# Kernel optimization log

Hardware: AMD Instinct MI355X
Metric: run time of the kernel (lower is better)

Reference implementation:

```python
import jax, jax.numpy as jnp
import numpy as np

N_AGENTS = 3
OBS_DIM = 30
ACT_DIM = 9
HIDDEN = 128
HEADS = 4
HEAD_DIM = HIDDEN // HEADS
BATCH = 131072
NEG_SLOPE = 0.01
MASK_VAL = -1e10


def _leaky(x):
    return jnp.where(x >= 0, x, NEG_SLOPE * x)


def setup_inputs() -> dict:
    key = jax.random.key(0)
    ks = jax.random.split(key, 20)

    def init(k, shape, fan_in):
        return jax.random.normal(k, shape, dtype=jnp.float32) / np.sqrt(fan_in)

    inp = {
        "observations": jax.random.normal(ks[0], (BATCH, N_AGENTS, OBS_DIM), dtype=jnp.float32),
        "actions": jax.random.uniform(ks[1], (BATCH, N_AGENTS, ACT_DIM), dtype=jnp.float32),
        # per-agent embed weights, stacked over agents: [N, in, out] (already transposed vs torch)
        "W_o": init(ks[2], (N_AGENTS, OBS_DIM, HIDDEN), OBS_DIM),
        "b_o": jnp.zeros((N_AGENTS, HIDDEN), dtype=jnp.float32),
        "W_oa": init(ks[3], (N_AGENTS, OBS_DIM + ACT_DIM, HIDDEN), OBS_DIM + ACT_DIM),
        "b_oa": jnp.zeros((N_AGENTS, HIDDEN), dtype=jnp.float32),
        # shared attention projections: [in, out]
        "Wq": init(ks[4], (HIDDEN, HIDDEN), HIDDEN),
        "bq": jnp.zeros((HIDDEN,), dtype=jnp.float32),
        "Wk": init(ks[5], (HIDDEN, HIDDEN), HIDDEN),
        "bk": jnp.zeros((HIDDEN,), dtype=jnp.float32),
        "Wv": init(ks[6], (HIDDEN, HIDDEN), HIDDEN),
        "bv": jnp.zeros((HIDDEN,), dtype=jnp.float32),
        # per-agent critic MLP: Linear(2H->H) + LeakyReLU + Linear(H->A)
        "Wc1": init(ks[7], (N_AGENTS, 2 * HIDDEN, HIDDEN), 2 * HIDDEN),
        "bc1": jnp.zeros((N_AGENTS, HIDDEN), dtype=jnp.float32),
        "Wc2": init(ks[8], (N_AGENTS, HIDDEN, ACT_DIM), HIDDEN),
        "bc2": jnp.zeros((N_AGENTS, ACT_DIM), dtype=jnp.float32),
    }
    return inp


def reference(observations, actions, W_o, b_o, W_oa, b_oa, Wq, bq, Wk, bk, Wv, bv, Wc1, bc1, Wc2, bc2):
    B, N, _ = observations.shape

    # per-agent embeds as a single batched GEMM over the agent axis
    o_emb = _leaky(jnp.einsum('bnd,ndh->bnh', observations, W_o) + b_o)          # [B,N,H]
    oa = jnp.concatenate([observations, actions], axis=-1)                        # [B,N,O+A]
    oa_emb = _leaky(jnp.einsum('bnd,ndh->bnh', oa, W_oa) + b_oa)                  # [B,N,H]

    # shared Q/K/V projections, split heads -> [B, heads, N, head_dim]
    def heads(x):
        return x.reshape(B, N, HEADS, HEAD_DIM).transpose(0, 2, 1, 3)

    Q = heads(o_emb @ Wq + bq)
    K = heads(oa_emb @ Wk + bk)
    V = heads(oa_emb @ Wv + bv)

    scores = jnp.einsum('bhnd,bhmd->bhnm', Q, K) / np.sqrt(HEAD_DIM).astype(np.float32)
    mask = jnp.where(jnp.eye(N, dtype=bool), jnp.float32(MASK_VAL), 0.0)          # diag masked
    attn = jax.nn.softmax(scores + mask, axis=-1)
    attn_out = jnp.einsum('bhnm,bhmd->bhnd', attn, V)
    attn_out = attn_out.transpose(0, 2, 1, 3).reshape(B, N, HIDDEN)               # [B,N,H]

    # per-agent critics, again batched over the agent axis
    c_in = jnp.concatenate([o_emb, attn_out], axis=-1)                            # [B,N,2H]
    h = _leaky(jnp.einsum('bnd,ndh->bnh', c_in, Wc1) + bc1)
    q_values = jnp.einsum('bnh,nha->bna', h, Wc2) + bc2                           # [B,N,A]
    return q_values
```

## Files before the change

kernel.cpp:

```cpp
#include <hip/hip_runtime.h>
#include <stdint.h>

typedef unsigned short u16;
typedef unsigned int u32;
typedef __attribute__((ext_vector_type(8))) short short8;
typedef __attribute__((ext_vector_type(4))) float floatx4;

#define BATCH   131072
#define NA      3
#define OBS     30
#define ACTD    9
#define HID     128
#define HEADS   4
#define HD      32
#define MB      16
#define ROWS    (MB*NA)
#define LDC     136
#define LDOA    72
#define QSCALE  0.17677669529663687f
#define NTHREADS 512

#define OFF_WO    0
#define OFF_WOA   12288
#define OFF_WQ    36864
#define OFF_WK    53248
#define OFF_WV    69632
#define OFF_WC1   86016
#define OFF_WC2   184320
#define PRE_TOTAL 190464

__device__ __forceinline__ u16 f2bf(float f) {
    union { float f; u32 u; } v; v.f = f;
    return (u16)((v.u + 0x8000u) >> 16);
}
__device__ __forceinline__ u32 pk_bf16(float a, float b) {
    union { float f; u32 u; } x, y; x.f = a; y.f = b;
    return ((x.u + 0x8000u) >> 16) | ((y.u + 0x8000u) & 0xffff0000u);
}
__device__ __forceinline__ float lo16f(u32 w) { union { u32 u; float f; } v; v.u = w << 16; return v.f; }
__device__ __forceinline__ float hi16f(u32 w) { union { u32 u; float f; } v; v.u = w & 0xffff0000u; return v.f; }
__device__ __forceinline__ float leaky(float x) { return x >= 0.f ? x : 0.01f * x; }

__global__ void prepack_kernel(const float* __restrict__ Wo,  const float* __restrict__ Woa,
                               const float* __restrict__ Wq,  const float* __restrict__ Wk,
                               const float* __restrict__ Wv,  const float* __restrict__ Wc1,
                               const float* __restrict__ Wc2, u16* __restrict__ out) {
    int i = blockIdx.x * blockDim.x + threadIdx.x;
    if (i >= PRE_TOTAL) return;
    const float* src; int K, KT, perA, base, Nsrc, Nlim; float scl = 1.f;
    if (i < OFF_WOA)      { src = Wo;  K = 30;  KT = 1; perA = 4096;  base = OFF_WO;  Nsrc = 128; Nlim = 128; }
    else if (i < OFF_WQ)  { src = Woa; K = 39;  KT = 2; perA = 8192;  base = OFF_WOA; Nsrc = 128; Nlim = 128; }
    else if (i < OFF_WK)  { src = Wq;  K = 128; KT = 4; perA = 16384; base = OFF_WQ;  Nsrc = 128; Nlim = 128; scl = QSCALE; }
    else if (i < OFF_WV)  { src = Wk;  K = 128; KT = 4; perA = 16384; base = OFF_WK;  Nsrc = 128; Nlim = 128; }
    else if (i < OFF_WC1) { src = Wv;  K = 128; KT = 4; perA = 16384; base = OFF_WV;  Nsrc = 128; Nlim = 128; }
    else if (i < OFF_WC2) { src = Wc1; K = 256; KT = 8; perA = 32768; base = OFF_WC1; Nsrc = 128; Nlim = 128; }
    else                  { src = Wc2; K = 128; KT = 4; perA = 2048;  base = OFF_WC2; Nsrc = 9;   Nlim = 9;   }
    int j = i - base;
    int agent = j / perA;
    int r = j - agent * perA;
    int e = r & 7, lane = (r >> 3) & 63, fk = r >> 9;
    int kt = fk % KT, nt = fk / KT;
    int n = nt * 16 + (lane & 15);
    int k = kt * 32 + (lane >> 4) * 8 + e;
    u16 v = 0;
    if (k < K && n < Nlim) v = f2bf(src[(agent * K + k) * Nsrc + n] * scl);
    out[i] = v;
}

__global__ __launch_bounds__(NTHREADS, 6) void fused_kernel(
    const float* __restrict__ obs, const float* __restrict__ act,
    const float* __restrict__ b_o, const float* __restrict__ b_oa,
    const float* __restrict__ bq,  const float* __restrict__ bk_, const float* __restrict__ bv,
    const float* __restrict__ bc1, const float* __restrict__ bc2,
    const u16* __restrict__ pre, float* __restrict__ out)
{
    __shared__ __align__(16) u16 s_mem[4 * ROWS * LDC];
    u16* s_oemb  = s_mem;
    u16* s_oaemb = s_mem + ROWS * LDC;
    u16* s_bufA  = s_mem + 2 * ROWS * LDC;
    u16* s_bufB  = s_mem + 3 * ROWS * LDC;

    const int tid  = threadIdx.x;
    const int wave = tid >> 6, lane = tid & 63;
    const int l15  = lane & 15, quad = lane >> 4;
    const int b0   = blockIdx.x * MB;
    const short8* preV = (const short8*)pre;

    for (int g = tid; g < ROWS * 15; g += NTHREADS) {
        int r = g / 15, s = g - r * 15;
        int n = r / MB, bl = r - n * MB;
        const float* src = &obs[((b0 + bl) * NA + n) * OBS + 2 * s];
        *(u32*)&s_bufA[n * (MB * LDOA) + bl * LDOA + 2 * s] = pk_bf16(src[0], src[1]);
    }
    for (int g = tid; g < ROWS * 5; g += NTHREADS) {
        int r = g / 5, s = g - r * 5;
        int n = r / MB, bl = r - n * MB;
        const float* src = &act[((b0 + bl) * NA + n) * ACTD + 2 * s];
        float v0 = src[0], v1 = (s < 4) ? src[1] : 0.f;
        *(u32*)&s_bufA[n * (MB * LDOA) + bl * LDOA + 30 + 2 * s] = pk_bf16(v0, v1);
    }
    for (int g = tid; g < ROWS * 12; g += NTHREADS) {
        int r = g / 12, s = g - r * 12;
        int n = r / MB, bl = r - n * MB;
        *(u32*)&s_bufA[n * (MB * LDOA) + bl * LDOA + 40 + 2 * s] = 0;
    }
    __syncthreads();

    for (int sj = wave; sj < 24; sj += 8) {
        int osel = sj / 12;
        int rem = sj % 12, agent = rem >> 2, nh2 = rem & 3;
        int KTn = osel ? 2 : 1;
        const float* bias = osel ? b_oa : b_o;
        int preBase = osel ? (OFF_WOA / 8 + agent * 1024) : (OFF_WO / 8 + agent * 512);
        floatx4 acc[2] = {};
        for (int kt = 0; kt < KTn; kt++) {
            short8 a = *(const short8*)&s_bufA[agent * (MB * LDOA) + l15 * LDOA + kt * 32 + quad * 8];
            #pragma unroll
            for (int n2 = 0; n2 < 2; n2++) {
                int nt = nh2 * 2 + n2;
                short8 b = preV[preBase + (nt * KTn + kt) * 64 + lane];
                acc[n2] = __builtin_amdgcn_mfma_f32_16x16x32_bf16(a, b, acc[n2], 0, 0, 0);
            }
        }
        u16* dst = osel ? s_oaemb : s_oemb;
        #pragma unroll
        for (int n2 = 0; n2 < 2; n2++) {
            int col = (nh2 * 2 + n2) * 16 + l15;
            float bb = bias[agent * HID + col];
            #pragma unroll
            for (int rg = 0; rg < 4; rg++) {
                int m = quad * 4 + rg;
                dst[(m * NA + agent) * LDC + col] = f2bf(leaky(acc[n2][rg] + bb));
            }
        }
    }
    __syncthreads();

    {
        int proj = wave >> 2, nh2 = wave & 3;
        const u16* Abuf = proj ? s_oaemb : s_oemb;
        int preBase = (proj ? OFF_WK : OFF_WQ) / 8;
        u16* dst = proj ? s_bufB : s_bufA;
        const float* bias = proj ? bk_ : bq;
        float bscl = proj ? 1.f : QSCALE;
        short8 wf[8];
        #pragma unroll
        for (int n2 = 0; n2 < 2; n2++)
            #pragma unroll
            for (int kt = 0; kt < 4; kt++)
                wf[n2 * 4 + kt] = preV[preBase + ((nh2 * 2 + n2) * 4 + kt) * 64 + lane];
        for (int mt = 0; mt < 3; mt++) {
            short8 xa[4];
            #pragma unroll
            for (int kt = 0; kt < 4; kt++)
                xa[kt] = *(const short8*)&Abuf[(mt * 16 + l15) * LDC + kt * 32 + quad * 8];
            floatx4 acc[2] = {};
            #pragma unroll
            for (int n2 = 0; n2 < 2; n2++)
                #pragma unroll
                for (int kt = 0; kt < 4; kt++)
                    acc[n2] = __builtin_amdgcn_mfma_f32_16x16x32_bf16(xa[kt], wf[n2 * 4 + kt], acc[n2], 0, 0, 0);
            #pragma unroll
            for (int n2 = 0; n2 < 2; n2++) {
                int col = (nh2 * 2 + n2) * 16 + l15;
                float bb = bias[col] * bscl;
                #pragma unroll
                for (int rg = 0; rg < 4; rg++) {
                    int m = mt * 16 + quad * 4 + rg;
                    dst[m * LDC + col] = f2bf(acc[n2][rg] + bb);
                }
            }
        }
    }
    __syncthreads();

    float2 prob = make_float2(0.f, 0.f);
    int e3 = 0, h3 = 0, n3 = 0, m30 = 0, m31 = 0;
    const bool attn_thread = (tid < MB * HEADS * NA);
    if (attn_thread) {
        int r = tid;
        e3 = r / (HEADS * NA); r -= e3 * HEADS * NA; h3 = r / NA; n3 = r - h3 * NA;
        m30 = (n3 == 0) ? 1 : 0;
        m31 = (n3 == 2) ? 1 : 2;
        const uint4* qp  = (const uint4*)&s_bufA[(e3 * NA + n3) * LDC + h3 * HD];
        const uint4* kp0 = (const uint4*)&s_bufB[(e3 * NA + m30) * LDC + h3 * HD];
        const uint4* kp1 = (const uint4*)&s_bufB[(e3 * NA + m31) * LDC + h3 * HD];
        float s0 = 0.f, s1 = 0.f;
        #pragma unroll
        for (int c = 0; c < 4; c++) {
            uint4 qw = qp[c], aw = kp0[c], bw = kp1[c];
            u32 qv[4] = {qw.x, qw.y, qw.z, qw.w};
            u32 av[4] = {aw.x, aw.y, aw.z, aw.w};
            u32 bv_[4] = {bw.x, bw.y, bw.z, bw.w};
            #pragma unroll
            for (int j = 0; j < 4; j++) {
                float ql = lo16f(qv[j]), qh = hi16f(qv[j]);
                s0 += ql * lo16f(av[j]) + qh * hi16f(av[j]);
                s1 += ql * lo16f(bv_[j]) + qh * hi16f(bv_[j]);
            }
        }
        float mx = fmaxf(s0, s1);
        float p0 = __expf(s0 - mx), p1 = __expf(s1 - mx);
        float inv = 1.f / (p0 + p1);
        prob = make_float2(p0 * inv, p1 * inv);
    }
    __syncthreads();

    {
        int nt = wave;
        short8 wf[4];
        #pragma unroll
        for (int kt = 0; kt < 4; kt++)
            wf[kt] = preV[OFF_WV / 8 + (nt * 4 + kt) * 64 + lane];
        for (int mt = 0; mt < 3; mt++) {
            short8 xa[4];
            #pragma unroll
            for (int kt = 0; kt < 4; kt++)
                xa[kt] = *(const short8*)&s_oaemb[(mt * 16 + l15) * LDC + kt * 32 + quad * 8];
            floatx4 acc = {};
            #pragma unroll
            for (int kt = 0; kt < 4; kt++)
                acc = __builtin_amdgcn_mfma_f32_16x16x32_bf16(xa[kt], wf[kt], acc, 0, 0, 0);
            int col = nt * 16 + l15;
            float bb = bv[col];
            #pragma unroll
            for (int rg = 0; rg < 4; rg++) {
                int m = mt * 16 + quad * 4 + rg;
                s_bufA[m * LDC + col] = f2bf(acc[rg] + bb);
            }
        }
    }
    __syncthreads();

    if (attn_thread) {
        const uint4* v0p = (const uint4*)&s_bufA[(e3 * NA + m30) * LDC + h3 * HD];
        const uint4* v1p = (const uint4*)&s_bufA[(e3 * NA + m31) * LDC + h3 * HD];
        uint4* dst = (uint4*)&s_oaemb[(e3 * NA + n3) * LDC + h3 * HD];
        #pragma unroll
        for (int c = 0; c < 4; c++) {
            uint4 aw = v0p[c], bw = v1p[c], ow;
            u32 av[4] = {aw.x, aw.y, aw.z, aw.w};
            u32 bv_[4] = {bw.x, bw.y, bw.z, bw.w};
            u32 ov[4];
            #pragma unroll
            for (int j = 0; j < 4; j++) {
                float lo = prob.x * lo16f(av[j]) + prob.y * lo16f(bv_[j]);
                float hi = prob.x * hi16f(av[j]) + prob.y * hi16f(bv_[j]);
                ov[j] = pk_bf16(lo, hi);
            }
            ow.x = ov[0]; ow.y = ov[1]; ow.z = ov[2]; ow.w = ov[3];
            dst[c] = ow;
        }
    }
    __syncthreads();

    for (int sj = wave; sj < 24; sj += 8) {
        int agent = sj >> 3, nt = sj & 7;
        floatx4 acc = {};
        for (int kt = 0; kt < 8; kt++) {
            const u16* A = (kt < 4) ? s_oemb : s_oaemb;
            int kk = (kt & 3) * 32 + quad * 8;
            short8 a = *(const short8*)&A[(l15 * NA + agent) * LDC + kk];
            short8 b = preV[OFF_WC1 / 8 + agent * 4096 + (nt * 8 + kt) * 64 + lane];
            acc = __builtin_amdgcn_mfma_f32_16x16x32_bf16(a, b, acc, 0, 0, 0);
        }
        int col = nt * 16 + l15;
        float bb = bc1[agent * HID + col];
        #pragma unroll
        for (int rg = 0; rg < 4; rg++) {
            int m = quad * 4 + rg;
            s_bufB[(m * NA + agent) * LDC + col] = f2bf(leaky(acc[rg] + bb));
        }
    }
    __syncthreads();

    if (wave < NA) {
        int agent = wave;
        floatx4 acc = {};
        #pragma unroll
        for (int kt = 0; kt < 4; kt++) {
            short8 a = *(const short8*)&s_bufB[(l15 * NA + agent) * LDC + kt * 32 + quad * 8];
            short8 b = preV[OFF_WC2 / 8 + agent * 256 + kt * 64 + lane];
            acc = __builtin_amdgcn_mfma_f32_16x16x32_bf16(a, b, acc, 0, 0, 0);
        }
        int col = l15;
        if (col < ACTD) {
            float bb = bc2[agent * ACTD + col];
            #pragma unroll
            for (int rg = 0; rg < 4; rg++) {
                int m = quad * 4 + rg;
                out[((b0 + m) * NA + agent) * ACTD + col] = acc[rg] + bb;
            }
        }
    }
}

extern "C" void kernel_launch(void* const* d_in, const int* in_sizes, int n_in,
                              void* d_out, int out_size, void* d_ws, size_t ws_size,
                              hipStream_t stream) {
    const float* obs = (const float*)d_in[0];
    const float* act = (const float*)d_in[1];
    const float* Wo  = (const float*)d_in[2];
    const float* bo  = (const float*)d_in[3];
    const float* Woa = (const float*)d_in[4];
    const float* boa = (const float*)d_in[5];
    const float* Wq  = (const float*)d_in[6];
    const float* bq  = (const float*)d_in[7];
    const float* Wk  = (const float*)d_in[8];
    const float* bk  = (const float*)d_in[9];
    const float* Wv  = (const float*)d_in[10];
    const float* bv  = (const float*)d_in[11];
    const float* Wc1 = (const float*)d_in[12];
    const float* bc1 = (const float*)d_in[13];
    const float* Wc2 = (const float*)d_in[14];
    const float* bc2 = (const float*)d_in[15];
    u16* pre = (u16*)d_ws;

    prepack_kernel<<<(PRE_TOTAL + 255) / 256, 256, 0, stream>>>(Wo, Woa, Wq, Wk, Wv, Wc1, Wc2, pre);
    fused_kernel<<<BATCH / MB, NTHREADS, 0, stream>>>(obs, act, bo, boa, bq, bk, bv, bc1, bc2, pre,
                                                      (float*)d_out);
}
```

Baseline: 261.8 us.

## Swap MFMA operands to emit transposed tiles with packed vector LDS stores

Every MFMA now takes weights as the A operand and activations as B, so each lane holds 4 consecutive output features for one row. Epilogues can then add a float4 bias and write one packed 8-byte LDS store instead of four scattered 2-byte stores. The V-projection and critic-1 stages are re-tiled so that 6 waves each reuse activation fragments across 4 output tiles, leaving 2 waves idle. Packing uses v_perm and leaky uses fmax. Together these aim to cut LDS store traffic and bank conflicts, at the cost of lower wave utilisation in those stages and more weight-fragment loads per wave.

```diff
diff --git a/kernel.cpp b/kernel.cpp
--- a/kernel.cpp
+++ b/kernel.cpp
@@ -33,13 +33,13 @@
     union { float f; u32 u; } v; v.f = f;
     return (u16)((v.u + 0x8000u) >> 16);
 }
-__device__ __forceinline__ u32 pk_bf16(float a, float b) {
+__device__ __forceinline__ u32 pk2(float a, float b) {
     union { float f; u32 u; } x, y; x.f = a; y.f = b;
-    return ((x.u + 0x8000u) >> 16) | ((y.u + 0x8000u) & 0xffff0000u);
+    return __builtin_amdgcn_perm(y.u + 0x8000u, x.u + 0x8000u, 0x07060302u);
 }
 __device__ __forceinline__ float lo16f(u32 w) { union { u32 u; float f; } v; v.u = w << 16; return v.f; }
 __device__ __forceinline__ float hi16f(u32 w) { union { u32 u; float f; } v; v.u = w & 0xffff0000u; return v.f; }
-__device__ __forceinline__ float leaky(float x) { return x >= 0.f ? x : 0.01f * x; }
+__device__ __forceinline__ float leaky(float x) { return fmaxf(x, 0.01f * x); }
 
 __global__ void prepack_kernel(const float* __restrict__ Wo,  const float* __restrict__ Woa,
                                const float* __restrict__ Wq,  const float* __restrict__ Wk,
@@ -90,14 +90,14 @@
         int r = g / 15, s = g - r * 15;
         int n = r / MB, bl = r - n * MB;
         const float* src = &obs[((b0 + bl) * NA + n) * OBS + 2 * s];
-        *(u32*)&s_bufA[n * (MB * LDOA) + bl * LDOA + 2 * s] = pk_bf16(src[0], src[1]);
+        *(u32*)&s_bufA[n * (MB * LDOA) + bl * LDOA + 2 * s] = pk2(src[0], src[1]);
     }
     for (int g = tid; g < ROWS * 5; g += NTHREADS) {
         int r = g / 5, s = g - r * 5;
         int n = r / MB, bl = r - n * MB;
         const float* src = &act[((b0 + bl) * NA + n) * ACTD + 2 * s];
         float v0 = src[0], v1 = (s < 4) ? src[1] : 0.f;
-        *(u32*)&s_bufA[n * (MB * LDOA) + bl * LDOA + 30 + 2 * s] = pk_bf16(v0, v1);
+        *(u32*)&s_bufA[n * (MB * LDOA) + bl * LDOA + 30 + 2 * s] = pk2(v0, v1);
     }
     for (int g = tid; g < ROWS * 12; g += NTHREADS) {
         int r = g / 12, s = g - r * 12;
@@ -110,28 +110,28 @@
         int osel = sj / 12;
         int rem = sj % 12, agent = rem >> 2, nh2 = rem & 3;
         int KTn = osel ? 2 : 1;
-        const float* bias = osel ? b_oa : b_o;
+        const float* bias = (osel ? b_oa : b_o) + agent * HID;
         int preBase = osel ? (OFF_WOA / 8 + agent * 1024) : (OFF_WO / 8 + agent * 512);
         floatx4 acc[2] = {};
         for (int kt = 0; kt < KTn; kt++) {
-            short8 a = *(const short8*)&s_bufA[agent * (MB * LDOA) + l15 * LDOA + kt * 32 + quad * 8];
+            short8 xb = *(const short8*)&s_bufA[agent * (MB * LDOA) + l15 * LDOA + kt * 32 + quad * 8];
             #pragma unroll
             for (int n2 = 0; n2 < 2; n2++) {
                 int nt = nh2 * 2 + n2;
-                short8 b = preV[preBase + (nt * KTn + kt) * 64 + lane];
-                acc[n2] = __builtin_amdgcn_mfma_f32_16x16x32_bf16(a, b, acc[n2], 0, 0, 0);
+                short8 wa = preV[preBase + (nt * KTn + kt) * 64 + lane];
+                acc[n2] = __builtin_amdgcn_mfma_f32_16x16x32_bf16(wa, xb, acc[n2], 0, 0, 0);
             }
         }
         u16* dst = osel ? s_oaemb : s_oemb;
+        int r = l15 * NA + agent;
         #pragma unroll
         for (int n2 = 0; n2 < 2; n2++) {
-            int col = (nh2 * 2 + n2) * 16 + l15;
-            float bb = bias[agent * HID + col];
-            #pragma unroll
-            for (int rg = 0; rg < 4; rg++) {
-                int m = quad * 4 + rg;
-                dst[(m * NA + agent) * LDC + col] = f2bf(leaky(acc[n2][rg] + bb));
-            }
+            int f0 = (nh2 * 2 + n2) * 16 + quad * 4;
+            float4 bb = *(const float4*)&bias[f0];
+            uint2 w;
+            w.x = pk2(leaky(acc[n2][0] + bb.x), leaky(acc[n2][1] + bb.y));
+            w.y = pk2(leaky(acc[n2][2] + bb.z), leaky(acc[n2][3] + bb.w));
+            *(uint2*)&dst[r * LDC + f0] = w;
         }
     }
     __syncthreads();
@@ -150,25 +150,25 @@
             for (int kt = 0; kt < 4; kt++)
                 wf[n2 * 4 + kt] = preV[preBase + ((nh2 * 2 + n2) * 4 + kt) * 64 + lane];
         for (int mt = 0; mt < 3; mt++) {
-            short8 xa[4];
+            short8 xb[4];
             #pragma unroll
             for (int kt = 0; kt < 4; kt++)
-                xa[kt] = *(const short8*)&Abuf[(mt * 16 + l15) * LDC + kt * 32 + quad * 8];
+                xb[kt] = *(const short8*)&Abuf[(mt * 16 + l15) * LDC + kt * 32 + quad * 8];
             floatx4 acc[2] = {};
             #pragma unroll
             for (int n2 = 0; n2 < 2; n2++)
                 #pragma unroll
                 for (int kt = 0; kt < 4; kt++)
-                    acc[n2] = __builtin_amdgcn_mfma_f32_16x16x32_bf16(xa[kt], wf[n2 * 4 + kt], acc[n2], 0, 0, 0);
+                    acc[n2] = __builtin_amdgcn_mfma_f32_16x16x32_bf16(wf[n2 * 4 + kt], xb[kt], acc[n2], 0, 0, 0);
+            int r = mt * 16 + l15;
             #pragma unroll
             for (int n2 = 0; n2 < 2; n2++) {
-                int col = (nh2 * 2 + n2) * 16 + l15;
-                float bb = bias[col] * bscl;
-                #pragma unroll
-                for (int rg = 0; rg < 4; rg++) {
-                    int m = mt * 16 + quad * 4 + rg;
-                    dst[m * LDC + col] = f2bf(acc[n2][rg] + bb);
-                }
+                int f0 = (nh2 * 2 + n2) * 16 + quad * 4;
+                float4 bb = *(const float4*)&bias[f0];
+                uint2 w;
+                w.x = pk2(acc[n2][0] + bb.x * bscl, acc[n2][1] + bb.y * bscl);
+                w.y = pk2(acc[n2][2] + bb.z * bscl, acc[n2][3] + bb.w * bscl);
+                *(uint2*)&dst[r * LDC + f0] = w;
             }
         }
     }
@@ -206,28 +206,28 @@
     }
     __syncthreads();
 
-    {
-        int nt = wave;
-        short8 wf[4];
+    for (int sj = wave; sj < 6; sj += 8) {
+        int mt = sj >> 1, nhalf = sj & 1;
+        short8 xb[4];
         #pragma unroll
         for (int kt = 0; kt < 4; kt++)
-            wf[kt] = preV[OFF_WV / 8 + (nt * 4 + kt) * 64 + lane];
-        for (int mt = 0; mt < 3; mt++) {
-            short8 xa[4];
-            #pragma unroll
-            for (int kt = 0; kt < 4; kt++)
-                xa[kt] = *(const short8*)&s_oaemb[(mt * 16 + l15) * LDC + kt * 32 + quad * 8];
+            xb[kt] = *(const short8*)&s_oaemb[(mt * 16 + l15) * LDC + kt * 32 + quad * 8];
+        int r = mt * 16 + l15;
+        #pragma unroll
+        for (int n4 = 0; n4 < 4; n4++) {
+            int nt = nhalf * 4 + n4;
             floatx4 acc = {};
             #pragma unroll
-            for (int kt = 0; kt < 4; kt++)
-                acc = __builtin_amdgcn_mfma_f32_16x16x32_bf16(xa[kt], wf[kt], acc, 0, 0, 0);
-            int col = nt * 16 + l15;
-            float bb = bv[col];
-            #pragma unroll
-            for (int rg = 0; rg < 4; rg++) {
-                int m = mt * 16 + quad * 4 + rg;
-                s_bufA[m * LDC + col] = f2bf(acc[rg] + bb);
-            }
+            for (int kt = 0; kt < 4; kt++) {
+                short8 wa = preV[OFF_WV / 8 + (nt * 4 + kt) * 64 + lane];
+                acc = __builtin_amdgcn_mfma_f32_16x16x32_bf16(wa, xb[kt], acc, 0, 0, 0);
+            }
+            int f0 = nt * 16 + quad * 4;
+            float4 bb = *(const float4*)&bv[f0];
+            uint2 w;
+            w.x = pk2(acc[0] + bb.x, acc[1] + bb.y);
+            w.y = pk2(acc[2] + bb.z, acc[3] + bb.w);
+            *(uint2*)&s_bufA[r * LDC + f0] = w;
         }
     }
     __syncthreads();
@@ -246,7 +246,7 @@
             for (int j = 0; j < 4; j++) {
                 float lo = prob.x * lo16f(av[j]) + prob.y * lo16f(bv_[j]);
                 float hi = prob.x * hi16f(av[j]) + prob.y * hi16f(bv_[j]);
-                ov[j] = pk_bf16(lo, hi);
+                ov[j] = pk2(lo, hi);
             }
             ow.x = ov[0]; ow.y = ov[1]; ow.z = ov[2]; ow.w = ov[3];
             dst[c] = ow;
@@ -254,43 +254,49 @@
     }
     __syncthreads();
 
-    for (int sj = wave; sj < 24; sj += 8) {
-        int agent = sj >> 3, nt = sj & 7;
-        floatx4 acc = {};
+    for (int sj = wave; sj < 6; sj += 8) {
+        int agent = sj >> 1, nhalf = sj & 1;
+        int r = l15 * NA + agent;
+        short8 xb[8];
+        #pragma unroll
         for (int kt = 0; kt < 8; kt++) {
             const u16* A = (kt < 4) ? s_oemb : s_oaemb;
-            int kk = (kt & 3) * 32 + quad * 8;
-            short8 a = *(const short8*)&A[(l15 * NA + agent) * LDC + kk];
-            short8 b = preV[OFF_WC1 / 8 + agent * 4096 + (nt * 8 + kt) * 64 + lane];
-            acc = __builtin_amdgcn_mfma_f32_16x16x32_bf16(a, b, acc, 0, 0, 0);
-        }
-        int col = nt * 16 + l15;
-        float bb = bc1[agent * HID + col];
-        #pragma unroll
-        for (int rg = 0; rg < 4; rg++) {
-            int m = quad * 4 + rg;
-            s_bufB[(m * NA + agent) * LDC + col] = f2bf(leaky(acc[rg] + bb));
+            xb[kt] = *(const short8*)&A[r * LDC + (kt & 3) * 32 + quad * 8];
+        }
+        #pragma unroll
+        for (int n4 = 0; n4 < 4; n4++) {
+            int nt = nhalf * 4 + n4;
+            floatx4 acc = {};
+            #pragma unroll
+            for (int kt = 0; kt < 8; kt++) {
+                short8 wa = preV[OFF_WC1 / 8 + agent * 4096 + (nt * 8 + kt) * 64 + lane];
+                acc = __builtin_amdgcn_mfma_f32_16x16x32_bf16(wa, xb[kt], acc, 0, 0, 0);
+            }
+            int f0 = nt * 16 + quad * 4;
+            float4 bb = *(const float4*)&bc1[agent * HID + f0];
+            uint2 w;
+            w.x = pk2(leaky(acc[0] + bb.x), leaky(acc[1] + bb.y));
+            w.y = pk2(leaky(acc[2] + bb.z), leaky(acc[3] + bb.w));
+            *(uint2*)&s_bufB[r * LDC + f0] = w;
         }
     }
     __syncthreads();
 
     if (wave < NA) {
         int agent = wave;
+        int r = l15 * NA + agent;
         floatx4 acc = {};
         #pragma unroll
         for (int kt = 0; kt < 4; kt++) {
-            short8 a = *(const short8*)&s_bufB[(l15 * NA + agent) * LDC + kt * 32 + quad * 8];
-            short8 b = preV[OFF_WC2 / 8 + agent * 256 + kt * 64 + lane];
-            acc = __builtin_amdgcn_mfma_f32_16x16x32_bf16(a, b, acc, 0, 0, 0);
-        }
-        int col = l15;
-        if (col < ACTD) {
-            float bb = bc2[agent * ACTD + col];
-            #pragma unroll
-            for (int rg = 0; rg < 4; rg++) {
-                int m = quad * 4 + rg;
-                out[((b0 + m) * NA + agent) * ACTD + col] = acc[rg] + bb;
-            }
+            short8 xb = *(const short8*)&s_bufB[r * LDC + kt * 32 + quad * 8];
+            short8 wa = preV[OFF_WC2 / 8 + agent * 256 + kt * 64 + lane];
+            acc = __builtin_amdgcn_mfma_f32_16x16x32_bf16(wa, xb, acc, 0, 0, 0);
+        }
+        #pragma unroll
+        for (int rg = 0; rg < 4; rg++) {
+            int a = quad * 4 + rg;
+            if (a < ACTD)
+                out[((size_t)(b0 + l15) * NA + agent) * ACTD + a] = acc[rg] + bc2[agent * ACTD + a];
         }
     }
 }
```

Result: slower. 297.3 us (+13.5%).
